# Optimization experiments

Hardware: AMD Instinct MI355X
Metric: run time of the kernel (lower is better)

The kernel has to match this reference:

```python
import jax, jax.numpy as jnp
import numpy as np

SPLIT_K = 64  # cfg.split_k; bilinear feature dim d = W_dim // SPLIT_K


def _per_doc(seq, att, ep, W_s, W_o, W_c, A_bl, b_bl, W_attn, v_attn, clf_W, clf_b):
    # seq [S,H], att [heads,S,S], ep [N,M] mention token positions
    # entity rep: logsumexp pooling over mention embeddings
    rep = jax.scipy.special.logsumexp(seq[ep], axis=1)                 # [N,H]
    # entity attention: sum of mention attention rows
    ga = att[:, ep, :].sum(axis=2).transpose(1, 0, 2)                  # [N,heads,S]
    # pairwise localized context: product of head-wise attentions, summed over heads
    pa = jnp.einsum('ihs,jhs->ijs', ga, ga)                            # [N,N,S]
    pa = pa / pa.sum(-1, keepdims=True)
    ctx = jnp.einsum('ijs,sh->ijh', pa, seq) @ W_c                     # [N,N,W]
    Zs = jnp.tanh((rep @ W_s)[:, None, :] + ctx)                       # [N,N,W]
    Zo = jnp.tanh((rep @ W_o)[:, None, :] + ctx)
    N, Wd = Zs.shape[0], Zs.shape[-1]
    d = Wd // SPLIT_K
    # torch: split into Wd//SPLIT_K chunks of size SPLIT_K, stack at -1 -> [N,N,SPLIT_K,d]
    Zs4 = Zs.reshape(N, N, d, SPLIT_K).swapaxes(-1, -2)
    Zo4 = Zo.reshape(N, N, d, SPLIT_K).swapaxes(-1, -2)
    # grouped bilinear scoring, summed over the SPLIT_K groups (bias added per group)
    g = jnp.einsum('ijkp,opq,ijkq->ijo', Zs4, A_bl, Zo4) + SPLIT_K * b_bl  # [N,N,W]
    # axis attention over the N x N pair grid: row-wise and column-wise softmax contexts
    e = jnp.tanh(g @ W_attn) @ v_attn                                  # [N,N]
    a_row = jax.nn.softmax(e, axis=1)
    a_col = jax.nn.softmax(e, axis=0)
    r = (g
         + jnp.einsum('ij,ijd->id', a_row, g)[:, None, :]
         + jnp.einsum('ij,ijd->jd', a_col, g)[None, :, :])
    return r @ clf_W + clf_b                                           # [N,N,num_class]


def setup_inputs() -> dict:
    key = jax.random.key(0)
    ks = jax.random.split(key, 12)
    B, S, H, Hh, N, M = 4, 1024, 768, 12, 32, 4
    Wd, AD, C = 768, 256, 97
    d = Wd // SPLIT_K
    p = lambda k, shape: jax.random.normal(k, shape, dtype=jnp.float32) * 0.02
    return {
        'sequence_output': jax.random.normal(ks[0], (B, S, H), dtype=jnp.float32),
        'attention': jax.random.uniform(ks[1], (B, Hh, S, S), dtype=jnp.float32),
        'entity_pos': jax.random.randint(ks[2], (B, N, M), 0, S),
        'W_s': p(ks[3], (H, Wd)),
        'W_o': p(ks[4], (H, Wd)),
        'W_c': p(ks[5], (H, Wd)),
        'A_bl': p(ks[6], (Wd, d, d)),
        'b_bl': p(ks[7], (Wd,)),
        'W_attn': p(ks[8], (Wd, AD)),
        'v_attn': p(ks[9], (AD,)),
        'clf_W': p(ks[10], (Wd, C)),
        'clf_b': p(ks[11], (C,)),
    }


def reference(sequence_output, attention, entity_pos, W_s, W_o, W_c, A_bl, b_bl,
              W_attn, v_attn, clf_W, clf_b):
    f = jax.vmap(_per_doc, in_axes=(0, 0, 0) + (None,) * 9)
    return f(sequence_output, attention, entity_pos, W_s, W_o, W_c, A_bl, b_bl,
             W_attn, v_attn, clf_W, clf_b)  # [B,N,N,num_class]
```

## Files before the change

kernel.cpp:

```cpp
#include <hip/hip_runtime.h>
#include <hip/hip_bf16.h>
#include <math.h>

#define BB 4
#define SS 1024
#define HH 768
#define NHEAD 12
#define NN 32
#define MM 4
#define WD 768
#define AD 256
#define NC 97
#define SPK 64
#define DD 12
#define KP 160

typedef __attribute__((ext_vector_type(8))) short short8;
typedef __attribute__((ext_vector_type(4))) short sshort4;
typedef __attribute__((ext_vector_type(4))) float float4_t;

__device__ inline unsigned short f2bf(float x) {
  union { float f; unsigned int u; } v; v.f = x;
  unsigned int r = v.u + 0x7fffu + ((v.u >> 16) & 1u);
  return (unsigned short)(r >> 16);
}
__device__ inline float bf2f(unsigned short x) {
  union { unsigned int u; float f; } v; v.u = ((unsigned int)x) << 16;
  return v.f;
}

__device__ __forceinline__ void gl_lds16(unsigned short* l, const unsigned short* g) {
  __builtin_amdgcn_global_load_lds(
      (const __attribute__((address_space(1))) unsigned int*)g,
      (__attribute__((address_space(3))) unsigned int*)l, 16, 0, 0);
}

__device__ __forceinline__ void transpose_tile(const float* __restrict__ in,
                                               unsigned short* __restrict__ out,
                                               int R, int C, int Cp, int t, int tilesR) {
  __shared__ float tile[32][33];
  int r0 = (t % tilesR) * 32, c0 = (t / tilesR) * 32;
  int tx = threadIdx.x & 31, ty = threadIdx.x >> 5;
#pragma unroll
  for (int i = 0; i < 32; i += 8) {
    int r = r0 + ty + i, c = c0 + tx;
    tile[ty + i][tx] = (c < C) ? in[(size_t)r * C + c] : 0.f;
  }
  __syncthreads();
#pragma unroll
  for (int i = 0; i < 32; i += 8) {
    int c = c0 + ty + i, r = r0 + tx;
    if (c < Cp) out[(size_t)c * R + r] = f2bf(tile[tx][ty + i]);
  }
}

__global__ __launch_bounds__(256) void k_front(
    const float* __restrict__ seq, const float* __restrict__ att,
    const int* __restrict__ ep, const float* __restrict__ W_c,
    const float* __restrict__ W_s, const float* __restrict__ W_o,
    const float* __restrict__ clf_W, const float* __restrict__ A_bl,
    const float* __restrict__ W_attn, const float* __restrict__ b_bl,
    unsigned short* __restrict__ gaB, unsigned short* __restrict__ FB,
    float* __restrict__ tb, float* __restrict__ ebuf,
    unsigned short* __restrict__ seqB, unsigned short* __restrict__ WcT,
    unsigned short* __restrict__ WsoT, unsigned short* __restrict__ clfT,
    unsigned short* __restrict__ AblB, unsigned short* __restrict__ repB) {
  int bid = blockIdx.x;
  int tid = threadIdx.x;
  if (bid < 1536) {
    int h = bid % NHEAD;
    int bn = bid / NHEAD;
    int b = bn / NN;
    const int* e = ep + (size_t)bn * MM;
    int i0 = e[0], i1 = e[1], i2 = e[2], i3 = e[3];
    const float* ab = att + ((size_t)b * NHEAD + h) * SS * SS;
    unsigned short* go = gaB + ((size_t)bn * NHEAD + h) * SS;
#pragma unroll
    for (int r = 0; r < 4; ++r) {
      int s = tid + r * 256;
      go[s] = f2bf(ab[(size_t)i0 * SS + s] + ab[(size_t)i1 * SS + s] +
                   ab[(size_t)i2 * SS + s] + ab[(size_t)i3 * SS + s]);
    }
    return;
  }
  bid -= 1536;
  if (bid < 256) {
    int a = bid;
    int k = tid;
    if (k < KP) {
      float acc = 0.f;
      if (k < DD * DD) {
        for (int w = 0; w < WD; ++w)
          acc += A_bl[(size_t)w * (DD * DD) + k] * W_attn[(size_t)w * AD + a];
      }
      FB[(size_t)a * KP + k] = f2bf(acc);
    }
    return;
  }
  bid -= 256;
  if (bid < 1) {
    int a = tid;
    float acc = 0.f;
    for (int w = 0; w < WD; ++w) acc += b_bl[w] * W_attn[(size_t)w * AD + a];
    tb[a] = (float)SPK * acc;
    return;
  }
  bid -= 1;
  if (bid < 16) {
    int idx = bid * 256 + tid;
    if (idx < BB * NN * NN) ebuf[idx] = 0.f;
    return;
  }
  bid -= 16;
  if (bid < 3072) {
    int i = (bid * 256 + tid) * 4;
    float4 v = *(const float4*)&seq[i];
    seqB[i + 0] = f2bf(v.x); seqB[i + 1] = f2bf(v.y);
    seqB[i + 2] = f2bf(v.z); seqB[i + 3] = f2bf(v.w);
    return;
  }
  bid -= 3072;
  if (bid < 576) { transpose_tile(W_c, WcT, HH, WD, WD, bid, 24); return; }
  bid -= 576;
  if (bid < 576) { transpose_tile(W_s, WsoT, HH, WD, WD, bid, 24); return; }
  bid -= 576;
  if (bid < 576) { transpose_tile(W_o, WsoT + (size_t)WD * HH, HH, WD, WD, bid, 24); return; }
  bid -= 576;
  if (bid < 96)  { transpose_tile(clf_W, clfT, WD, NC, 128, bid, 24); return; }
  bid -= 96;
  if (bid < 480) {
    int idx = bid * 256 + tid;
    int w = idx / KP, pq = idx % KP;
    AblB[idx] = (pq < DD * DD) ? f2bf(A_bl[(size_t)w * DD * DD + pq]) : 0;
    return;
  }
  bid -= 480;
  {
    int bn = bid; int b = bn / NN;
    const int* e = ep + (size_t)bn * MM;
    int i0 = e[0], i1 = e[1], i2 = e[2], i3 = e[3];
    const float* sb = seq + (size_t)b * SS * HH;
    for (int h = tid; h < HH; h += 256) {
      float v0 = sb[(size_t)i0 * HH + h];
      float v1 = sb[(size_t)i1 * HH + h];
      float v2 = sb[(size_t)i2 * HH + h];
      float v3 = sb[(size_t)i3 * HH + h];
      float mx = fmaxf(fmaxf(v0, v1), fmaxf(v2, v3));
      float s = expf(v0 - mx) + expf(v1 - mx) + expf(v2 - mx) + expf(v3 - mx);
      repB[(size_t)bn * HH + h] = f2bf(mx + logf(s));
    }
  }
}

__global__ __launch_bounds__(256) void k_pa(const unsigned short* __restrict__ gaB,
                                            unsigned short* __restrict__ pa) {
  int t = blockIdx.x;
  int j = t % NN;
  int i = (t / NN) % NN;
  int b = t / (NN * NN);
  const unsigned short* gi = gaB + ((size_t)(b * NN + i)) * NHEAD * SS;
  const unsigned short* gj = gaB + ((size_t)(b * NN + j)) * NHEAD * SS;
  int s0 = threadIdx.x * 4;
  float acc[4] = {0.f, 0.f, 0.f, 0.f};
#pragma unroll
  for (int h = 0; h < NHEAD; ++h) {
    sshort4 a4 = *(const sshort4*)&gi[h * SS + s0];
    sshort4 b4 = *(const sshort4*)&gj[h * SS + s0];
#pragma unroll
    for (int r = 0; r < 4; ++r)
      acc[r] += bf2f((unsigned short)a4[r]) * bf2f((unsigned short)b4[r]);
  }
  float tot = acc[0] + acc[1] + acc[2] + acc[3];
  __shared__ float red[256];
  red[threadIdx.x] = tot;
  __syncthreads();
  for (int o = 128; o > 0; o >>= 1) {
    if (threadIdx.x < o) red[threadIdx.x] += red[threadIdx.x + o];
    __syncthreads();
  }
  float inv = 1.0f / red[0];
  unsigned short ov[4];
#pragma unroll
  for (int r = 0; r < 4; ++r) ov[r] = f2bf(acc[r] * inv);
  *(sshort4*)&pa[(size_t)t * SS + s0] = *(sshort4*)ov;
}

template <int MODE>
__global__ __launch_bounds__(256)
void k_mm(const unsigned short* __restrict__ A, const unsigned short* __restrict__ B,
          void* __restrict__ Cv, int Nc, int K, int ldb, int ldc,
          long long sA, long long sB, long long sC,
          const float* __restrict__ bias, float biasScale,
          const float* __restrict__ rcWp, const float* __restrict__ clf_b) {
  A += (long long)blockIdx.z * sA;
  B += (long long)blockIdx.z * sB;
  __shared__ __align__(16) unsigned short As[128 * 32];
  __shared__ __align__(16) unsigned short Bs[128 * 32];
  const int tid = threadIdx.x;
  const int m0 = blockIdx.y * 128;
  const int n0 = blockIdx.x * 128;
  const int lane = tid & 63;
  const int w = tid >> 6;
  const int wr = (w >> 1) * 64, wc = (w & 1) * 64;
  const int q = lane >> 4, l16 = lane & 15;
  const int lr = lane >> 2, lq = lane & 3;
  float4_t acc[4][4] = {};
  const unsigned short* Ag0 = A + (size_t)(m0 + w * 16 + lr) * K + lq * 8;
  const unsigned short* Ag1 = Ag0 + (size_t)64 * K;
  const unsigned short* Bg0 = B + (size_t)(n0 + w * 16 + lr) * ldb + lq * 8;
  const unsigned short* Bg1 = Bg0 + (size_t)64 * ldb;
  unsigned short* Al0 = &As[(w * 16) * 32];
  unsigned short* Al1 = &As[(64 + w * 16) * 32];
  unsigned short* Bl0 = &Bs[(w * 16) * 32];
  unsigned short* Bl1 = &Bs[(64 + w * 16) * 32];
  for (int k0 = 0; k0 < K; k0 += 32) {
    gl_lds16(Al0, Ag0 + k0);
    gl_lds16(Al1, Ag1 + k0);
    gl_lds16(Bl0, Bg0 + k0);
    gl_lds16(Bl1, Bg1 + k0);
    __syncthreads();
    short8 af[4], bfr[4];
#pragma unroll
    for (int i = 0; i < 4; ++i)
      af[i] = *(const short8*)&As[(wr + i * 16 + l16) * 32 + q * 8];
#pragma unroll
    for (int j = 0; j < 4; ++j)
      bfr[j] = *(const short8*)&Bs[(wc + j * 16 + l16) * 32 + q * 8];
#pragma unroll
    for (int i = 0; i < 4; ++i)
#pragma unroll
      for (int j = 0; j < 4; ++j)
        acc[i][j] = __builtin_amdgcn_mfma_f32_16x16x32_bf16(af[i], bfr[j], acc[i][j], 0, 0, 0);
    __syncthreads();
  }
  if (MODE == 4) {
    float* ep = (float*)Cv;
#pragma unroll
    for (int i = 0; i < 4; ++i) {
#pragma unroll
      for (int r = 0; r < 4; ++r) {
        float part = 0.f;
#pragma unroll
        for (int j = 0; j < 4; ++j) {
          int n = n0 + wc + j * 16 + l16;
          float v = acc[i][j][r] + bias[n];
          part += tanhf(v) * rcWp[n];
        }
#pragma unroll
        for (int d = 1; d < 16; d <<= 1) part += __shfl_xor(part, d, 16);
        if (l16 == 0) atomicAdd(&ep[m0 + wr + i * 16 + q * 4 + r], part);
      }
    }
    return;
  }
  float* Cf = (float*)Cv + (long long)blockIdx.z * sC;
  unsigned short* Cb = (unsigned short*)Cv + (long long)blockIdx.z * sC;
#pragma unroll
  for (int i = 0; i < 4; ++i) {
    int mbase = m0 + wr + i * 16 + q * 4;
#pragma unroll
    for (int j = 0; j < 4; ++j) {
      int n = n0 + wc + j * 16 + l16;
      if (n < Nc) {
        float badd = bias ? biasScale * bias[n] : 0.f;
#pragma unroll
        for (int r = 0; r < 4; ++r) {
          int m = mbase + r;
          float v = acc[i][j][r] + badd;
          if (MODE == 3) {
            int b = m >> 10, ii = (m >> 5) & 31, jj = m & 31;
            v += rcWp[(size_t)(b * NN + ii) * NC + n] +
                 rcWp[(size_t)(BB * NN + b * NN + jj) * NC + n] + clf_b[n];
          }
          if (MODE == 1)      Cb[(size_t)m * ldc + n] = f2bf(v);
          else if (MODE == 2) Cf[(size_t)n * ldc + m] = v;
          else                Cf[(size_t)m * ldc + n] = v;
        }
      }
    }
  }
}

__global__ __launch_bounds__(256) void k_M(const unsigned short* __restrict__ ctx,
                                           const float* __restrict__ rso,
                                           unsigned short* __restrict__ Mm) {
  int t = blockIdx.x;
  const float* rsi = rso + (size_t)(t >> 5) * 1536;
  __shared__ float zsT[64 * 13];
  __shared__ float zoT[64 * 13];
  const unsigned short* cx = ctx + (size_t)t * WD;
  for (int wd = threadIdx.x; wd < WD; wd += blockDim.x) {
    float c = bf2f(cx[wd]);
    int k = wd & 63, p = wd >> 6;
    zsT[k * 13 + p] = tanhf(rsi[wd] + c);
    zoT[k * 13 + p] = tanhf(rsi[WD + wd] + c);
  }
  __syncthreads();
  int pq = threadIdx.x;
  if (pq < KP) {
    float s = 0.f;
    if (pq < DD * DD) {
      int p = pq / DD, qq = pq % DD;
#pragma unroll
      for (int k = 0; k < SPK; ++k) s += zsT[k * 13 + p] * zoT[k * 13 + qq];
    }
    Mm[(size_t)t * KP + pq] = f2bf(s);
  }
}

__global__ __launch_bounds__(256) void k_rowcolW(const float* __restrict__ e,
                                                 const unsigned short* __restrict__ g,
                                                 const float* __restrict__ clf_W,
                                                 float* __restrict__ rcW) {
  int t = blockIdx.x;
  int which = t >> 7;
  int bn = t & 127;
  int b = bn >> 5, x = bn & 31;
  int tid = threadIdx.x;
  __shared__ float av[NN];
  __shared__ float rcs[WD];
  if (tid < NN)
    av[tid] = (which == 0) ? e[(size_t)b * 1024 + x * NN + tid]
                           : e[(size_t)b * 1024 + tid * NN + x];
  __syncthreads();
  float mx = -1e30f;
#pragma unroll 8
  for (int k = 0; k < NN; ++k) mx = fmaxf(mx, av[k]);
  float sm = 0.f;
  float wk[NN];
#pragma unroll 8
  for (int k = 0; k < NN; ++k) { wk[k] = expf(av[k] - mx); sm += wk[k]; }
  float inv = 1.0f / sm;
  const unsigned short* gb = g + (size_t)b * 1024 * WD;
  for (int o = tid; o < WD; o += 256) {
    float s = 0.f;
#pragma unroll 8
    for (int k = 0; k < NN; ++k) {
      int pair = (which == 0) ? x * NN + k : k * NN + x;
      s += wk[k] * bf2f(gb[(size_t)pair * WD + o]);
    }
    rcs[o] = s * inv;
  }
  __syncthreads();
  if (tid < NC) {
    float s = 0.f;
    for (int o = 0; o < WD; ++o) s += rcs[o] * clf_W[(size_t)o * NC + tid];
    rcW[(size_t)(which * 128 + bn) * NC + tid] = s;
  }
}

extern "C" void kernel_launch(void* const* d_in, const int* in_sizes, int n_in,
                              void* d_out, int out_size, void* d_ws, size_t ws_size,
                              hipStream_t stream) {
  const float* seq    = (const float*)d_in[0];
  const float* att    = (const float*)d_in[1];
  const int*   ep     = (const int*)d_in[2];
  const float* W_s    = (const float*)d_in[3];
  const float* W_o    = (const float*)d_in[4];
  const float* W_c    = (const float*)d_in[5];
  const float* A_bl   = (const float*)d_in[6];
  const float* b_bl   = (const float*)d_in[7];
  const float* W_attn = (const float*)d_in[8];
  const float* v_attn = (const float*)d_in[9];
  const float* clf_W  = (const float*)d_in[10];
  const float* clf_b  = (const float*)d_in[11];
  float* out = (float*)d_out;

  char* base = (char*)d_ws;
  size_t off = 0;
  auto alloc = [&](size_t bytes) {
    char* p = base + off;
    off += (bytes + 255) & ~(size_t)255;
    return p;
  };
  unsigned short* repB = (unsigned short*)alloc((size_t)BB * NN * HH * 2);
  float* rso  = (float*)alloc((size_t)BB * NN * 2 * WD * 4);
  unsigned short* gaB  = (unsigned short*)alloc((size_t)BB * NN * NHEAD * SS * 2);
  unsigned short* paB  = (unsigned short*)alloc((size_t)BB * NN * NN * SS * 2);
  unsigned short* seqB = (unsigned short*)alloc((size_t)BB * SS * HH * 2);
  unsigned short* WcT  = (unsigned short*)alloc((size_t)HH * WD * 2);
  unsigned short* clfT = (unsigned short*)alloc((size_t)128 * WD * 2);
  unsigned short* WsoT = (unsigned short*)alloc((size_t)2 * WD * HH * 2);
  unsigned short* scT  = (unsigned short*)alloc((size_t)WD * BB * SS * 2);
  unsigned short* ctxB = (unsigned short*)alloc((size_t)BB * NN * NN * WD * 2);
  unsigned short* MmB  = (unsigned short*)alloc((size_t)BB * NN * NN * KP * 2);
  unsigned short* AblB = (unsigned short*)alloc((size_t)WD * KP * 2);
  unsigned short* FB   = (unsigned short*)alloc((size_t)AD * KP * 2);
  float* tb   = (float*)alloc((size_t)AD * 4);
  float* ebuf = (float*)alloc((size_t)BB * NN * NN * 4);
  float* rcW  = (float*)alloc((size_t)2 * BB * NN * NC * 4);
  unsigned short* gB = paB;

  const float* nof = nullptr;

  k_front<<<dim3(7313), dim3(256), 0, stream>>>(
      seq, att, ep, W_c, W_s, W_o, clf_W, A_bl, W_attn, b_bl,
      gaB, FB, tb, ebuf, seqB, WcT, WsoT, clfT, AblB, repB);

  k_mm<1><<<dim3(BB * SS / 128, WD / 128, 1), dim3(256), 0, stream>>>(
      WcT, seqB, scT, BB * SS, HH, HH, BB * SS, 0LL, 0LL, 0LL, nof, 0.f, nof, nof);

  k_mm<2><<<dim3(1, 12, 1), dim3(256), 0, stream>>>(
      WsoT, repB, rso, BB * NN, HH, HH, 2 * WD, 0LL, 0LL, 0LL, nof, 0.f, nof, nof);

  k_pa<<<dim3(BB * NN * NN), dim3(256), 0, stream>>>(gaB, paB);

  k_mm<1><<<dim3(WD / 128, NN * NN / 128, BB), dim3(256), 0, stream>>>(
      paB, scT, ctxB, WD, SS, BB * SS, WD,
      (long long)NN * NN * SS, (long long)SS, (long long)NN * NN * WD,
      nof, 0.f, nof, nof);

  k_M<<<dim3(BB * NN * NN), dim3(256), 0, stream>>>(ctxB, rso, MmB);

  k_mm<4><<<dim3(AD / 128, BB * NN * NN / 128, 1), dim3(256), 0, stream>>>(
      MmB, FB, ebuf, AD, KP, KP, 0, 0LL, 0LL, 0LL, tb, 1.f, v_attn, nof);

  k_mm<1><<<dim3(WD / 128, BB * NN * NN / 128, 1), dim3(256), 0, stream>>>(
      MmB, AblB, gB, WD, KP, KP, WD, 0LL, 0LL, 0LL, b_bl, (float)SPK, nof, nof);

  k_rowcolW<<<dim3(2 * BB * NN), dim3(256), 0, stream>>>(ebuf, gB, clf_W, rcW);

  k_mm<3><<<dim3(1, BB * NN * NN / 128, 1), dim3(256), 0, stream>>>(
      gB, clfT, out, NC, WD, WD, NC, 0LL, 0LL, 0LL, nof, 0.f, rcW, clf_b);
}
```

Before: 468.8 us.

## Fold classifier into bilinear weights and merge GEMMs into fewer fused launches

Precomputes clf_W·A_bl and the folded bias so the final classifier GEMM over g becomes part of one concatenated GEMM on MmB, which produces g, the attention energies and the base logits in a single launch. The row and column context terms are added to the output with atomics, which removes the separate classifier GEMM and the rcW buffer. The pa computation and the two projection GEMMs are merged into one launch, and all GEMMs move to 64x64 tiles for more blocks. The cost is many atomicAdds on the output, an ordering dependency that requires out to be written before the atomics, and smaller tiles with less reuse.

```diff
diff --git a/kernel.cpp b/kernel.cpp
--- a/kernel.cpp
+++ b/kernel.cpp
@@ -54,17 +54,52 @@
   }
 }
 
+__device__ __forceinline__ void gemm64(
+    const unsigned short* __restrict__ A, int lda,
+    const unsigned short* __restrict__ B, int ldb, int K,
+    int m0, int n0, unsigned short* As, unsigned short* Bs,
+    float4_t acc[2][2]) {
+  const int tid = threadIdx.x;
+  const int lane = tid & 63;
+  const int w = tid >> 6;
+  const int lr = lane >> 2, lq = lane & 3;
+  const unsigned short* Ag = A + (size_t)(m0 + w * 16 + lr) * lda + lq * 8;
+  const unsigned short* Bg = B + (size_t)(n0 + w * 16 + lr) * ldb + lq * 8;
+  unsigned short* Al = &As[(w * 16) * 32];
+  unsigned short* Bl = &Bs[(w * 16) * 32];
+  const int wr2 = (w >> 1) * 32, wc2 = (w & 1) * 32;
+  const int q = lane >> 4, l16 = lane & 15;
+  for (int k0 = 0; k0 < K; k0 += 32) {
+    gl_lds16(Al, Ag + k0);
+    gl_lds16(Bl, Bg + k0);
+    __syncthreads();
+    short8 af[2], bfr[2];
+#pragma unroll
+    for (int i = 0; i < 2; ++i)
+      af[i] = *(const short8*)&As[(wr2 + i * 16 + l16) * 32 + q * 8];
+#pragma unroll
+    for (int j = 0; j < 2; ++j)
+      bfr[j] = *(const short8*)&Bs[(wc2 + j * 16 + l16) * 32 + q * 8];
+#pragma unroll
+    for (int i = 0; i < 2; ++i)
+#pragma unroll
+      for (int j = 0; j < 2; ++j)
+        acc[i][j] = __builtin_amdgcn_mfma_f32_16x16x32_bf16(af[i], bfr[j], acc[i][j], 0, 0, 0);
+    __syncthreads();
+  }
+}
+
 __global__ __launch_bounds__(256) void k_front(
     const float* __restrict__ seq, const float* __restrict__ att,
     const int* __restrict__ ep, const float* __restrict__ W_c,
     const float* __restrict__ W_s, const float* __restrict__ W_o,
-    const float* __restrict__ clf_W, const float* __restrict__ A_bl,
-    const float* __restrict__ W_attn, const float* __restrict__ b_bl,
-    unsigned short* __restrict__ gaB, unsigned short* __restrict__ FB,
-    float* __restrict__ tb, float* __restrict__ ebuf,
+    const float* __restrict__ clf_W, const float* __restrict__ clf_b,
+    const float* __restrict__ A_bl, const float* __restrict__ W_attn,
+    const float* __restrict__ b_bl,
+    unsigned short* __restrict__ gaB, unsigned short* __restrict__ BcatB,
+    float* __restrict__ tb, float* __restrict__ tb2, float* __restrict__ ebuf,
     unsigned short* __restrict__ seqB, unsigned short* __restrict__ WcT,
-    unsigned short* __restrict__ WsoT, unsigned short* __restrict__ clfT,
-    unsigned short* __restrict__ AblB, unsigned short* __restrict__ repB) {
+    unsigned short* __restrict__ WsoT, unsigned short* __restrict__ repB) {
   int bid = blockIdx.x;
   int tid = threadIdx.x;
   if (bid < 1536) {
@@ -85,24 +120,49 @@
   }
   bid -= 1536;
   if (bid < 256) {
-    int a = bid;
-    int k = tid;
+    int a = bid, k = tid;
     if (k < KP) {
       float acc = 0.f;
       if (k < DD * DD) {
         for (int w = 0; w < WD; ++w)
           acc += A_bl[(size_t)w * (DD * DD) + k] * W_attn[(size_t)w * AD + a];
       }
-      FB[(size_t)a * KP + k] = f2bf(acc);
+      BcatB[(size_t)(768 + a) * KP + k] = f2bf(acc);
     }
     return;
   }
   bid -= 256;
+  if (bid < 128) {
+    int c = bid, k = tid;
+    if (k < KP) {
+      float acc = 0.f;
+      if (k < DD * DD && c < NC) {
+        for (int o = 0; o < WD; ++o)
+          acc += clf_W[(size_t)o * NC + c] * A_bl[(size_t)o * (DD * DD) + k];
+      }
+      BcatB[(size_t)(1024 + c) * KP + k] = f2bf(acc);
+    }
+    return;
+  }
+  bid -= 128;
   if (bid < 1) {
     int a = tid;
     float acc = 0.f;
     for (int w = 0; w < WD; ++w) acc += b_bl[w] * W_attn[(size_t)w * AD + a];
     tb[a] = (float)SPK * acc;
+    return;
+  }
+  bid -= 1;
+  if (bid < 1) {
+    int c = tid;
+    if (c < 128) {
+      float acc = 0.f;
+      if (c < NC) {
+        for (int o = 0; o < WD; ++o) acc += b_bl[o] * clf_W[(size_t)o * NC + c];
+        acc = (float)SPK * acc + clf_b[c];
+      }
+      tb2[c] = acc;
+    }
     return;
   }
   bid -= 1;
@@ -126,12 +186,10 @@
   bid -= 576;
   if (bid < 576) { transpose_tile(W_o, WsoT + (size_t)WD * HH, HH, WD, WD, bid, 24); return; }
   bid -= 576;
-  if (bid < 96)  { transpose_tile(clf_W, clfT, WD, NC, 128, bid, 24); return; }
-  bid -= 96;
   if (bid < 480) {
     int idx = bid * 256 + tid;
     int w = idx / KP, pq = idx % KP;
-    AblB[idx] = (pq < DD * DD) ? f2bf(A_bl[(size_t)w * DD * DD + pq]) : 0;
+    BcatB[idx] = (pq < DD * DD) ? f2bf(A_bl[(size_t)w * DD * DD + pq]) : 0;
     return;
   }
   bid -= 480;
@@ -152,133 +210,112 @@
   }
 }
 
-__global__ __launch_bounds__(256) void k_pa(const unsigned short* __restrict__ gaB,
-                                            unsigned short* __restrict__ pa) {
-  int t = blockIdx.x;
-  int j = t % NN;
-  int i = (t / NN) % NN;
-  int b = t / (NN * NN);
-  const unsigned short* gi = gaB + ((size_t)(b * NN + i)) * NHEAD * SS;
-  const unsigned short* gj = gaB + ((size_t)(b * NN + j)) * NHEAD * SS;
-  int s0 = threadIdx.x * 4;
-  float acc[4] = {0.f, 0.f, 0.f, 0.f};
-#pragma unroll
-  for (int h = 0; h < NHEAD; ++h) {
-    sshort4 a4 = *(const sshort4*)&gi[h * SS + s0];
-    sshort4 b4 = *(const sshort4*)&gj[h * SS + s0];
-#pragma unroll
-    for (int r = 0; r < 4; ++r)
-      acc[r] += bf2f((unsigned short)a4[r]) * bf2f((unsigned short)b4[r]);
-  }
-  float tot = acc[0] + acc[1] + acc[2] + acc[3];
-  __shared__ float red[256];
-  red[threadIdx.x] = tot;
-  __syncthreads();
-  for (int o = 128; o > 0; o >>= 1) {
-    if (threadIdx.x < o) red[threadIdx.x] += red[threadIdx.x + o];
+__global__ __launch_bounds__(256) void k_mid(
+    const unsigned short* __restrict__ gaB, unsigned short* __restrict__ paB,
+    const unsigned short* __restrict__ WcT, const unsigned short* __restrict__ seqB,
+    unsigned short* __restrict__ scT,
+    const unsigned short* __restrict__ WsoT, const unsigned short* __restrict__ repB,
+    float* __restrict__ rso) {
+  __shared__ __align__(16) unsigned short As[64 * 32];
+  __shared__ __align__(16) unsigned short Bs[64 * 32];
+  int bid = blockIdx.x;
+  int tid = threadIdx.x;
+  if (bid < 1024) {
+    int t = bid;
+    int j = t % NN;
+    int i = (t / NN) % NN;
+    int b = t / (NN * NN);
+    const unsigned short* gi = gaB + ((size_t)(b * NN + i)) * NHEAD * SS;
+    const unsigned short* gj = gaB + ((size_t)(b * NN + j)) * NHEAD * SS;
+    int s0 = tid * 4;
+    float acc[4] = {0.f, 0.f, 0.f, 0.f};
+#pragma unroll
+    for (int h = 0; h < NHEAD; ++h) {
+      sshort4 a4 = *(const sshort4*)&gi[h * SS + s0];
+      sshort4 b4 = *(const sshort4*)&gj[h * SS + s0];
+#pragma unroll
+      for (int r = 0; r < 4; ++r)
+        acc[r] += bf2f((unsigned short)a4[r]) * bf2f((unsigned short)b4[r]);
+    }
+    float tot = acc[0] + acc[1] + acc[2] + acc[3];
+    float* red = (float*)As;
+    red[tid] = tot;
     __syncthreads();
-  }
-  float inv = 1.0f / red[0];
-  unsigned short ov[4];
-#pragma unroll
-  for (int r = 0; r < 4; ++r) ov[r] = f2bf(acc[r] * inv);
-  *(sshort4*)&pa[(size_t)t * SS + s0] = *(sshort4*)ov;
-}
-
-template <int MODE>
-__global__ __launch_bounds__(256)
-void k_mm(const unsigned short* __restrict__ A, const unsigned short* __restrict__ B,
-          void* __restrict__ Cv, int Nc, int K, int ldb, int ldc,
-          long long sA, long long sB, long long sC,
-          const float* __restrict__ bias, float biasScale,
-          const float* __restrict__ rcWp, const float* __restrict__ clf_b) {
-  A += (long long)blockIdx.z * sA;
-  B += (long long)blockIdx.z * sB;
-  __shared__ __align__(16) unsigned short As[128 * 32];
-  __shared__ __align__(16) unsigned short Bs[128 * 32];
+    for (int o = 128; o > 0; o >>= 1) {
+      if (tid < o) red[tid] += red[tid + o];
+      __syncthreads();
+    }
+    float inv = 1.0f / red[0];
+    unsigned short ov[4];
+#pragma unroll
+    for (int r = 0; r < 4; ++r) ov[r] = f2bf(acc[r] * inv);
+    *(sshort4*)&paB[(size_t)t * SS + s0] = *(sshort4*)ov;
+    return;
+  }
+  const int lane = tid & 63, w = tid >> 6;
+  const int wr2 = (w >> 1) * 32, wc2 = (w & 1) * 32;
+  const int q = lane >> 4, l16 = lane & 15;
+  float4_t acc[2][2] = {};
+  if (bid < 1024 + 768) {
+    int b2 = bid - 1024;
+    int m0 = (b2 >> 6) * 64, n0 = (b2 & 63) * 64;
+    gemm64(WcT, HH, seqB, HH, HH, m0, n0, As, Bs, acc);
+#pragma unroll
+    for (int i = 0; i < 2; ++i)
+#pragma unroll
+      for (int j = 0; j < 2; ++j)
+#pragma unroll
+        for (int r = 0; r < 4; ++r) {
+          int m = m0 + wr2 + i * 16 + q * 4 + r;
+          int n = n0 + wc2 + j * 16 + l16;
+          scT[(size_t)m * (BB * SS) + n] = f2bf(acc[i][j][r]);
+        }
+    return;
+  }
+  {
+    int b3 = bid - 1792;
+    int m0 = (b3 >> 1) * 64, n0 = (b3 & 1) * 64;
+    gemm64(WsoT, HH, repB, HH, HH, m0, n0, As, Bs, acc);
+#pragma unroll
+    for (int i = 0; i < 2; ++i)
+#pragma unroll
+      for (int j = 0; j < 2; ++j)
+#pragma unroll
+        for (int r = 0; r < 4; ++r) {
+          int m = m0 + wr2 + i * 16 + q * 4 + r;
+          int n = n0 + wc2 + j * 16 + l16;
+          rso[(size_t)n * 1536 + m] = acc[i][j][r];
+        }
+  }
+}
+
+__global__ __launch_bounds__(256) void k_ctx(
+    const unsigned short* __restrict__ paB, const unsigned short* __restrict__ scT,
+    unsigned short* __restrict__ ctxB) {
+  __shared__ __align__(16) unsigned short As[64 * 32];
+  __shared__ __align__(16) unsigned short Bs[64 * 32];
+  int bid = blockIdx.x;
+  int doc = bid / 192;
+  int r2 = bid % 192;
+  int n0 = (r2 % 12) * 64, m0 = (r2 / 12) * 64;
   const int tid = threadIdx.x;
-  const int m0 = blockIdx.y * 128;
-  const int n0 = blockIdx.x * 128;
-  const int lane = tid & 63;
-  const int w = tid >> 6;
-  const int wr = (w >> 1) * 64, wc = (w & 1) * 64;
+  const int lane = tid & 63, w = tid >> 6;
+  const int wr2 = (w >> 1) * 32, wc2 = (w & 1) * 32;
   const int q = lane >> 4, l16 = lane & 15;
-  const int lr = lane >> 2, lq = lane & 3;
-  float4_t acc[4][4] = {};
-  const unsigned short* Ag0 = A + (size_t)(m0 + w * 16 + lr) * K + lq * 8;
-  const unsigned short* Ag1 = Ag0 + (size_t)64 * K;
-  const unsigned short* Bg0 = B + (size_t)(n0 + w * 16 + lr) * ldb + lq * 8;
-  const unsigned short* Bg1 = Bg0 + (size_t)64 * ldb;
-  unsigned short* Al0 = &As[(w * 16) * 32];
-  unsigned short* Al1 = &As[(64 + w * 16) * 32];
-  unsigned short* Bl0 = &Bs[(w * 16) * 32];
-  unsigned short* Bl1 = &Bs[(64 + w * 16) * 32];
-  for (int k0 = 0; k0 < K; k0 += 32) {
-    gl_lds16(Al0, Ag0 + k0);
-    gl_lds16(Al1, Ag1 + k0);
-    gl_lds16(Bl0, Bg0 + k0);
-    gl_lds16(Bl1, Bg1 + k0);
-    __syncthreads();
-    short8 af[4], bfr[4];
-#pragma unroll
-    for (int i = 0; i < 4; ++i)
-      af[i] = *(const short8*)&As[(wr + i * 16 + l16) * 32 + q * 8];
-#pragma unroll
-    for (int j = 0; j < 4; ++j)
-      bfr[j] = *(const short8*)&Bs[(wc + j * 16 + l16) * 32 + q * 8];
-#pragma unroll
-    for (int i = 0; i < 4; ++i)
-#pragma unroll
-      for (int j = 0; j < 4; ++j)
-        acc[i][j] = __builtin_amdgcn_mfma_f32_16x16x32_bf16(af[i], bfr[j], acc[i][j], 0, 0, 0);
-    __syncthreads();
-  }
-  if (MODE == 4) {
-    float* ep = (float*)Cv;
-#pragma unroll
-    for (int i = 0; i < 4; ++i) {
+  float4_t acc[2][2] = {};
+  gemm64(paB + (size_t)doc * SS * SS, SS, scT + (size_t)doc * SS, BB * SS, SS,
+         m0, n0, As, Bs, acc);
+  unsigned short* cb = ctxB + (size_t)doc * SS * WD;
+#pragma unroll
+  for (int i = 0; i < 2; ++i)
+#pragma unroll
+    for (int j = 0; j < 2; ++j)
 #pragma unroll
       for (int r = 0; r < 4; ++r) {
-        float part = 0.f;
-#pragma unroll
-        for (int j = 0; j < 4; ++j) {
-          int n = n0 + wc + j * 16 + l16;
-          float v = acc[i][j][r] + bias[n];
-          part += tanhf(v) * rcWp[n];
-        }
-#pragma unroll
-        for (int d = 1; d < 16; d <<= 1) part += __shfl_xor(part, d, 16);
-        if (l16 == 0) atomicAdd(&ep[m0 + wr + i * 16 + q * 4 + r], part);
-      }
-    }
-    return;
-  }
-  float* Cf = (float*)Cv + (long long)blockIdx.z * sC;
-  unsigned short* Cb = (unsigned short*)Cv + (long long)blockIdx.z * sC;
-#pragma unroll
-  for (int i = 0; i < 4; ++i) {
-    int mbase = m0 + wr + i * 16 + q * 4;
-#pragma unroll
-    for (int j = 0; j < 4; ++j) {
-      int n = n0 + wc + j * 16 + l16;
-      if (n < Nc) {
-        float badd = bias ? biasScale * bias[n] : 0.f;
-#pragma unroll
-        for (int r = 0; r < 4; ++r) {
-          int m = mbase + r;
-          float v = acc[i][j][r] + badd;
-          if (MODE == 3) {
-            int b = m >> 10, ii = (m >> 5) & 31, jj = m & 31;
-            v += rcWp[(size_t)(b * NN + ii) * NC + n] +
-                 rcWp[(size_t)(BB * NN + b * NN + jj) * NC + n] + clf_b[n];
-          }
-          if (MODE == 1)      Cb[(size_t)m * ldc + n] = f2bf(v);
-          else if (MODE == 2) Cf[(size_t)n * ldc + m] = v;
-          else                Cf[(size_t)m * ldc + n] = v;
-        }
-      }
-    }
-  }
+        int m = m0 + wr2 + i * 16 + q * 4 + r;
+        int n = n0 + wc2 + j * 16 + l16;
+        cb[(size_t)m * WD + n] = f2bf(acc[i][j][r]);
+      }
 }
 
 __global__ __launch_bounds__(256) void k_M(const unsigned short* __restrict__ ctx,
@@ -308,10 +345,74 @@
   }
 }
 
+__global__ __launch_bounds__(256) void k_eg(
+    const unsigned short* __restrict__ MmB, const unsigned short* __restrict__ BcatB,
+    unsigned short* __restrict__ gB, float* __restrict__ ebuf,
+    float* __restrict__ out, const float* __restrict__ b_bl,
+    const float* __restrict__ tb, const float* __restrict__ tb2,
+    const float* __restrict__ v_attn) {
+  __shared__ __align__(16) unsigned short As[64 * 32];
+  __shared__ __align__(16) unsigned short Bs[64 * 32];
+  int bid = blockIdx.x;
+  int n0 = (bid % 18) * 64, m0 = (bid / 18) * 64;
+  const int tid = threadIdx.x;
+  const int lane = tid & 63, w = tid >> 6;
+  const int wr2 = (w >> 1) * 32, wc2 = (w & 1) * 32;
+  const int q = lane >> 4, l16 = lane & 15;
+  float4_t acc[2][2] = {};
+  gemm64(MmB, KP, BcatB, KP, KP, m0, n0, As, Bs, acc);
+  if (n0 < 768) {
+#pragma unroll
+    for (int i = 0; i < 2; ++i)
+#pragma unroll
+      for (int j = 0; j < 2; ++j) {
+        int n = n0 + wc2 + j * 16 + l16;
+        float badd = (float)SPK * b_bl[n];
+#pragma unroll
+        for (int r = 0; r < 4; ++r) {
+          int m = m0 + wr2 + i * 16 + q * 4 + r;
+          gB[(size_t)m * WD + n] = f2bf(acc[i][j][r] + badd);
+        }
+      }
+  } else if (n0 < 1024) {
+#pragma unroll
+    for (int i = 0; i < 2; ++i) {
+#pragma unroll
+      for (int r = 0; r < 4; ++r) {
+        float part = 0.f;
+#pragma unroll
+        for (int j = 0; j < 2; ++j) {
+          int a = n0 - 768 + wc2 + j * 16 + l16;
+          part += tanhf(acc[i][j][r] + tb[a]) * v_attn[a];
+        }
+#pragma unroll
+        for (int d = 1; d < 16; d <<= 1) part += __shfl_xor(part, d, 16);
+        if (l16 == 0)
+          atomicAdd(&ebuf[m0 + wr2 + i * 16 + q * 4 + r], part);
+      }
+    }
+  } else {
+#pragma unroll
+    for (int i = 0; i < 2; ++i)
+#pragma unroll
+      for (int j = 0; j < 2; ++j) {
+        int c = n0 - 1024 + wc2 + j * 16 + l16;
+        if (c < NC) {
+          float badd = tb2[c];
+#pragma unroll
+          for (int r = 0; r < 4; ++r) {
+            int m = m0 + wr2 + i * 16 + q * 4 + r;
+            out[(size_t)m * NC + c] = acc[i][j][r] + badd;
+          }
+        }
+      }
+  }
+}
+
 __global__ __launch_bounds__(256) void k_rowcolW(const float* __restrict__ e,
                                                  const unsigned short* __restrict__ g,
                                                  const float* __restrict__ clf_W,
-                                                 float* __restrict__ rcW) {
+                                                 float* __restrict__ out) {
   int t = blockIdx.x;
   int which = t >> 7;
   int bn = t & 127;
@@ -345,7 +446,15 @@
   if (tid < NC) {
     float s = 0.f;
     for (int o = 0; o < WD; ++o) s += rcs[o] * clf_W[(size_t)o * NC + tid];
-    rcW[(size_t)(which * 128 + bn) * NC + tid] = s;
+    if (which == 0) {
+      float* ob = out + ((size_t)(b * NN + x) * NN) * NC + tid;
+#pragma unroll 4
+      for (int jj = 0; jj < NN; ++jj) atomicAdd(&ob[(size_t)jj * NC], s);
+    } else {
+      float* ob = out + ((size_t)(b * NN) * NN + x) * NC + tid;
+#pragma unroll 4
+      for (int ii = 0; ii < NN; ++ii) atomicAdd(&ob[(size_t)ii * NN * NC], s);
+    }
   }
 }
 
@@ -379,47 +488,29 @@
   unsigned short* paB  = (unsigned short*)alloc((size_t)BB * NN * NN * SS * 2);
   unsigned short* seqB = (unsigned short*)alloc((size_t)BB * SS * HH * 2);
   unsigned short* WcT  = (unsigned short*)alloc((size_t)HH * WD * 2);
-  unsigned short* clfT = (unsigned short*)alloc((size_t)128 * WD * 2);
   unsigned short* WsoT = (unsigned short*)alloc((size_t)2 * WD * HH * 2);
   unsigned short* scT  = (unsigned short*)alloc((size_t)WD * BB * SS * 2);
   unsigned short* ctxB = (unsigned short*)alloc((size_t)BB * NN * NN * WD * 2);
   unsigned short* MmB  = (unsigned short*)alloc((size_t)BB * NN * NN * KP * 2);
-  unsigned short* AblB = (unsigned short*)alloc((size_t)WD * KP * 2);
-  unsigned short* FB   = (unsigned short*)alloc((size_t)AD * KP * 2);
+  unsigned short* BcatB= (unsigned short*)alloc((size_t)1152 * KP * 2);
   float* tb   = (float*)alloc((size_t)AD * 4);
+  float* tb2  = (float*)alloc((size_t)128 * 4);
   float* ebuf = (float*)alloc((size_t)BB * NN * NN * 4);
-  float* rcW  = (float*)alloc((size_t)2 * BB * NN * NC * 4);
   unsigned short* gB = paB;
 
-  const float* nof = nullptr;
-
-  k_front<<<dim3(7313), dim3(256), 0, stream>>>(
-      seq, att, ep, W_c, W_s, W_o, clf_W, A_bl, W_attn, b_bl,
-      gaB, FB, tb, ebuf, seqB, WcT, WsoT, clfT, AblB, repB);
-
-  k_mm<1><<<dim3(BB * SS / 128, WD / 128, 1), dim3(256), 0, stream>>>(
-      WcT, seqB, scT, BB * SS, HH, HH, BB * SS, 0LL, 0LL, 0LL, nof, 0.f, nof, nof);
-
-  k_mm<2><<<dim3(1, 12, 1), dim3(256), 0, stream>>>(
-      WsoT, repB, rso, BB * NN, HH, HH, 2 * WD, 0LL, 0LL, 0LL, nof, 0.f, nof, nof);
-
-  k_pa<<<dim3(BB * NN * NN), dim3(256), 0, stream>>>(gaB, paB);
-
-  k_mm<1><<<dim3(WD / 128, NN * NN / 128, BB), dim3(256), 0, stream>>>(
-      paB, scT, ctxB, WD, SS, BB * SS, WD,
-      (long long)NN * NN * SS, (long long)SS, (long long)NN * NN * WD,
-      nof, 0.f, nof, nof);
+  k_front<<<dim3(7346), dim3(256), 0, stream>>>(
+      seq, att, ep, W_c, W_s, W_o, clf_W, clf_b, A_bl, W_attn, b_bl,
+      gaB, BcatB, tb, tb2, ebuf, seqB, WcT, WsoT, repB);
+
+  k_mid<<<dim3(1840), dim3(256), 0, stream>>>(
+      gaB, paB, WcT, seqB, scT, WsoT, repB, rso);
+
+  k_ctx<<<dim3(768), dim3(256), 0, stream>>>(paB, scT, ctxB);
 
   k_M<<<dim3(BB * NN * NN), dim3(256), 0, stream>>>(ctxB, rso, MmB);
 
-  k_mm<4><<<dim3(AD / 128, BB * NN * NN / 128, 1), dim3(256), 0, stream>>>(
-      MmB, FB, ebuf, AD, KP, KP, 0, 0LL, 0LL, 0LL, tb, 1.f, v_attn, nof);
-
-  k_mm<1><<<dim3(WD / 128, BB * NN * NN / 128, 1), dim3(256), 0, stream>>>(
-      MmB, AblB, gB, WD, KP, KP, WD, 0LL, 0LL, 0LL, b_bl, (float)SPK, nof, nof);
-
-  k_rowcolW<<<dim3(2 * BB * NN), dim3(256), 0, stream>>>(ebuf, gB, clf_W, rcW);
-
-  k_mm<3><<<dim3(1, BB * NN * NN / 128, 1), dim3(256), 0, stream>>>(
-      gB, clfT, out, NC, WD, WD, NC, 0LL, 0LL, 0LL, nof, 0.f, rcW, clf_b);
-}
+  k_eg<<<dim3(1152), dim3(256), 0, stream>>>(
+      MmB, BcatB, gB, ebuf, out, b_bl, tb, tb2, v_attn);
+
+  k_rowcolW<<<dim3(2 * BB * NN), dim3(256), 0, stream>>>(ebuf, gB, clf_W, out);
+}
```

After: 408.1 us. -13.0%, faster.
